# Optimization experiments

Measured on AMD Instinct MI355X. Metric: run time of the kernel, lower is better.

The kernel has to match this reference:

```python
import jax, jax.numpy as jnp
import numpy as np

B, T, I, H, O = 128, 512, 64, 1024, 12

def setup_inputs() -> dict:
    key = jax.random.key(0)
    ks = jax.random.split(key, 7)
    s_ih = 1.0 / np.sqrt(H)
    return {
        "x": jax.random.normal(ks[0], (B, T, I), dtype=jnp.float32),
        "W_ih": jax.random.normal(ks[1], (H, I), dtype=jnp.float32) * s_ih,
        "W_hh": jax.random.normal(ks[2], (H, H), dtype=jnp.float32) * s_ih,
        "b_ih": jax.random.normal(ks[3], (H,), dtype=jnp.float32) * s_ih,
        "b_hh": jax.random.normal(ks[4], (H,), dtype=jnp.float32) * s_ih,
        "W_out": jax.random.normal(ks[5], (O, H), dtype=jnp.float32) * s_ih,
        "b_out": jax.random.normal(ks[6], (O,), dtype=jnp.float32) * s_ih,
    }

def reference(x, W_ih, W_hh, b_ih, b_hh, W_out, b_out):
    # x: [B, T, I] (batch_first). Vanilla tanh RNN, h0 = 0.
    Bn, Tn, _ = x.shape
    Hn = W_hh.shape[0]
    # Precompute input projections for all timesteps (batched GEMM).
    xp = jnp.einsum('bti,hi->tbh', x, W_ih) + b_ih + b_hh  # [T, B, H]
    h0 = jnp.zeros((Bn, Hn), dtype=x.dtype)

    def step(h, xt):
        h_new = jnp.tanh(xt + h @ W_hh.T)
        return h_new, h_new

    _, hs = jax.lax.scan(step, h0, xp)  # hs: [T, B, H]
    hs = jnp.swapaxes(hs, 0, 1)         # [B, T, H]
    out = jnp.einsum('bth,oh->bto', hs, W_out) + b_out  # [B, T, O]
    return out.reshape(-1, 12)
```

## Files before the change

### kernel.cpp

```cpp
#include <hip/hip_runtime.h>
#include <hip/hip_bf16.h>

#define B_ 128
#define T_ 512
#define I_ 64
#define H_ 1024
#define O_ 12
#define HSTEP (H_ * B_)
#define XSTEP (I_ * B_)
#define RSLOT 16384
#define TIMEOUT 2000

typedef __attribute__((ext_vector_type(8))) short bf16x8;
typedef __attribute__((ext_vector_type(4))) float f32x4;

#define MFMA16 __builtin_amdgcn_mfma_f32_16x16x32_bf16

__device__ __forceinline__ float bf2f(unsigned short s) {
  unsigned u = ((unsigned)s) << 16; float f; __builtin_memcpy(&f, &u, 4); return f;
}
__device__ __forceinline__ unsigned short f2bf(float f) {
  unsigned u; __builtin_memcpy(&u, &f, 4);
  u += 0x7fffu + ((u >> 16) & 1u);
  return (unsigned short)(u >> 16);
}

__device__ __forceinline__ unsigned ldA32(const unsigned* p) {
  return __hip_atomic_load(p, __ATOMIC_RELAXED, __HIP_MEMORY_SCOPE_AGENT);
}
__device__ __forceinline__ void stA32(unsigned* p, unsigned v) {
  __hip_atomic_store(p, v, __ATOMIC_RELAXED, __HIP_MEMORY_SCOPE_AGENT);
}
__device__ __forceinline__ unsigned long long ldA64(const unsigned long long* p) {
  return __hip_atomic_load(p, __ATOMIC_RELAXED, __HIP_MEMORY_SCOPE_AGENT);
}

__device__ __forceinline__ void store32_sc0(unsigned* p, unsigned v) {
  asm volatile("global_store_dword %0, %1, off sc0" :: "v"(p), "v"(v) : "memory");
}
__device__ __forceinline__ unsigned poll_sc0(const unsigned* p) {
  unsigned v;
  asm volatile("global_load_dword %0, %1, off sc0\n\ts_waitcnt vmcnt(0)"
               : "=v"(v) : "v"(p) : "memory");
  return v;
}
__device__ __forceinline__ bf16x8 load16_sc0(const void* p) {
  bf16x8 v;
  asm volatile("global_load_dwordx4 %0, %1, off sc0" : "=v"(v) : "v"(p));
  return v;
}
__device__ __forceinline__ void waitv8(bf16x8& v0, bf16x8& v1, bf16x8& v2, bf16x8& v3,
                                       bf16x8& v4, bf16x8& v5, bf16x8& v6, bf16x8& v7) {
  asm volatile("s_waitcnt vmcnt(0)"
               : "+v"(v0), "+v"(v1), "+v"(v2), "+v"(v3),
                 "+v"(v4), "+v"(v5), "+v"(v6), "+v"(v7) :: "memory");
}

__global__ void prep_xp(const float* __restrict__ x,
                        unsigned short* __restrict__ xPhi) {
  const int t = blockIdx.x;
  for (int u = threadIdx.x; u < 1024; u += 256) {
    const int ib = u >> 7, b = u & 127;
    const float* src = x + ((size_t)b * T_ + t) * I_ + ib * 8;
    bf16x8 hi;
    #pragma unroll
    for (int j = 0; j < 8; ++j) hi[j] = (short)f2bf(src[j]);
    *(bf16x8*)(xPhi + ((size_t)t * 1024 + u) * 8) = hi;
  }
}

__global__ void prep_misc(const float* __restrict__ W_out, float* __restrict__ WoT,
                          unsigned* __restrict__ bar) {
  const int idx = blockIdx.x * 256 + threadIdx.x;
  if (idx < 1024) bar[idx] = 0u;
  const int k = idx >> 4, s = idx & 15;
  float v = 0.0f;
  if (s < 6)                 v = W_out[s * H_ + k];
  else if (s >= 8 && s < 14) v = W_out[(s - 2) * H_ + k];
  WoT[idx] = v;
}

__global__ __launch_bounds__(256, 1) void rnn_mfma(
    const float* __restrict__ W_ih, const float* __restrict__ W_hh,
    const float* __restrict__ b_ih, const float* __restrict__ b_hh,
    const unsigned short* __restrict__ xPhi, unsigned short* __restrict__ hP,
    unsigned short* __restrict__ rF, unsigned short* __restrict__ rS,
    unsigned* __restrict__ bar)
{
  __shared__ float part[4][544];
  __shared__ float biasS[32];
  __shared__ unsigned modeS;
  const int tid = threadIdx.x, bid = blockIdx.x;
  const int wave = tid >> 6, lane = tid & 63, quad = lane >> 4, ln = lane & 15;
  const int g = bid & 7, rg = bid >> 3;
  const int r0 = rg * 32, b0 = g * 16;
  if (tid < 32) biasS[tid] = b_ih[r0 + tid] + b_hh[r0 + tid];
  if (tid == 0) modeS = 1u;

  bf16x8 ahhi[2][8], ahlo[2][8];
  #pragma unroll
  for (int mt = 0; mt < 2; ++mt)
    #pragma unroll
    for (int kt = 0; kt < 8; ++kt) {
      const float* wp = W_hh + (size_t)(r0 + mt * 16 + ln) * H_
                        + wave * 256 + kt * 32 + quad * 8;
      #pragma unroll
      for (int j = 0; j < 8; ++j) {
        float v = wp[j];
        unsigned short h = f2bf(v);
        ahhi[mt][kt][j] = (short)h;
        ahlo[mt][kt][j] = (short)f2bf(v - bf2f(h));
      }
    }
  bf16x8 axhi[2], axlo[2];
  if (wave < 2)
    #pragma unroll
    for (int mt = 0; mt < 2; ++mt) {
      const float* wp = W_ih + (size_t)(r0 + mt * 16 + ln) * I_
                        + wave * 32 + quad * 8;
      #pragma unroll
      for (int j = 0; j < 8; ++j) {
        float v = wp[j];
        unsigned short h = f2bf(v);
        axhi[mt][j] = (short)h;
        axlo[mt][j] = (short)f2bf(v - bf2f(h));
      }
    }
  __syncthreads();
  unsigned mode = 1u;

  const int bcol = b0 + ln;
  unsigned short* rFg = rF + (size_t)g * 2 * RSLOT;
  unsigned short* rSg = rS + (size_t)g * 2 * RSLOT;

  f32x4 xacc0 = {0.f, 0.f, 0.f, 0.f}, xacc1 = {0.f, 0.f, 0.f, 0.f};
  auto computeX = [&](int t) {
    if (wave < 2) {
      const size_t xo = (((size_t)t * 8 + wave * 4 + quad) * B_ + bcol) * 8;
      bf16x8 bxh = *(const bf16x8*)(xPhi + xo);
      f32x4 t0 = {0.f, 0.f, 0.f, 0.f}, t1 = {0.f, 0.f, 0.f, 0.f};
      t0 = MFMA16(axhi[0], bxh, t0, 0, 0, 0);
      t0 = MFMA16(axlo[0], bxh, t0, 0, 0, 0);
      t1 = MFMA16(axhi[1], bxh, t1, 0, 0, 0);
      t1 = MFMA16(axlo[1], bxh, t1, 0, 0, 0);
      xacc0 = t0; xacc1 = t1;
    }
  };
  computeX(0);

  for (int t = 0; t < T_; ++t) {
    f32x4 accA0 = xacc0, accA1 = xacc1;
    f32x4 accB0 = {0.f, 0.f, 0.f, 0.f}, accB1 = {0.f, 0.f, 0.f, 0.f};

    if (t > 0) {
      const int soff = ((wave * 32 + quad) * 16 + ln) * 8;
      bf16x8 bh[8];
      if (mode) {
        const unsigned short* slot = rFg + ((t - 1) & 1) * RSLOT + soff;
        #pragma unroll
        for (int kt = 0; kt < 8; ++kt)
          bh[kt] = load16_sc0(slot + kt * 512);
        waitv8(bh[0], bh[1], bh[2], bh[3], bh[4], bh[5], bh[6], bh[7]);
      } else {
        const unsigned long long* slot =
            (const unsigned long long*)(rSg + ((t - 1) & 1) * RSLOT + soff);
        #pragma unroll
        for (int kt = 0; kt < 8; ++kt) {
          union { unsigned long long u[2]; bf16x8 v; } U;
          U.u[0] = ldA64(slot + kt * 128);
          U.u[1] = ldA64(slot + kt * 128 + 1);
          bh[kt] = U.v;
        }
      }
      #pragma unroll
      for (int kt = 0; kt < 8; ++kt) {
        accA0 = MFMA16(ahhi[0][kt], bh[kt], accA0, 0, 0, 0);
        accA1 = MFMA16(ahhi[1][kt], bh[kt], accA1, 0, 0, 0);
        accB0 = MFMA16(ahlo[0][kt], bh[kt], accB0, 0, 0, 0);
        accB1 = MFMA16(ahlo[1][kt], bh[kt], accB1, 0, 0, 0);
      }
    }

    #pragma unroll
    for (int r = 0; r < 4; ++r) {
      part[wave][r * 68 + lane]       = accA0[r] + accB0[r];
      part[wave][(4 + r) * 68 + lane] = accA1[r] + accB1[r];
    }
    __syncthreads();

    {
      const int n = tid & 15, rp = tid >> 4;
      const int m0 = rp * 2;
      unsigned short o[2];
      #pragma unroll
      for (int rr = 0; rr < 2; ++rr) {
        const int m = m0 + rr;
        const int f = ((m >> 4) * 4 + (m & 3)) * 68 + ((m >> 2) & 3) * 16 + n;
        float s = part[0][f] + part[1][f] + part[2][f] + part[3][f] + biasS[m];
        o[rr] = f2bf(tanhf(s));
      }
      const unsigned pk = (unsigned)o[0] | ((unsigned)o[1] << 16);
      const int R = r0 + m0;
      *(unsigned*)(hP + (size_t)t * HSTEP
                   + ((size_t)(R >> 3) * B_ + (b0 + n)) * 8 + (R & 7)) = pk;
      const int soff = ((R >> 3) * 16 + n) * 8 + (R & 7);
      store32_sc0((unsigned*)(rFg + (t & 1) * RSLOT + soff), pk);
      stA32      ((unsigned*)(rSg + (t & 1) * RSLOT + soff), pk);
    }

    if (t < T_ - 1) {
      computeX(t + 1);
      asm volatile("s_waitcnt vmcnt(0)" ::: "memory");
      __syncthreads();
      if (tid == 0) {
        store32_sc0(&bar[g * 32 + rg],      (unsigned)(t + 1));
        stA32      (&bar[256 + g * 32 + rg], (unsigned)(t + 1));
      }
      if (tid < 64) {
        int ok = 0;
        if (mode) {
          for (int it = 0; it < TIMEOUT && !ok; ++it) {
            unsigned v = (lane < 32) ? poll_sc0(&bar[g * 32 + lane]) : 0xffffffffu;
            ok = __all((int)(v >= (unsigned)(t + 1)));
          }
        }
        if (!ok) {
          if (tid == 0) modeS = 0u;
          for (;;) {
            unsigned v = (lane < 32) ? ldA32(&bar[256 + g * 32 + lane]) : 0xffffffffu;
            if (__all((int)(v >= (unsigned)(t + 1)))) break;
            __builtin_amdgcn_s_sleep(1);
          }
        }
      }
      __syncthreads();
      mode = modeS;
    }
  }
}

__global__ __launch_bounds__(256, 2) void out_proj(
    const unsigned short* __restrict__ hP, const float* __restrict__ WoT,
    const float* __restrict__ b_out, float* __restrict__ out)
{
  const int t = blockIdx.x;
  const int tid = threadIdx.x;
  const int b  = tid & 127;
  const int oh = tid >> 7;
  float a0 = b_out[oh * 6 + 0], a1 = b_out[oh * 6 + 1], a2 = b_out[oh * 6 + 2];
  float a3 = b_out[oh * 6 + 3], a4 = b_out[oh * 6 + 4], a5 = b_out[oh * 6 + 5];
  const unsigned short* hp = hP + (size_t)t * HSTEP + (size_t)b * 8;
  const float4* W4 = (const float4*)WoT;
  for (int kb = 0; kb < 128; ++kb) {
    bf16x8 hv = *(const bf16x8*)(hp + (size_t)kb * (B_ * 8));
    #pragma unroll
    for (int j = 0; j < 8; ++j) {
      const int k = kb * 8 + j;
      float h = bf2f((unsigned short)hv[j]);
      float4 wa = W4[k * 4 + oh * 2];
      float4 wb = W4[k * 4 + oh * 2 + 1];
      a0 += wa.x * h; a1 += wa.y * h; a2 += wa.z * h;
      a3 += wa.w * h; a4 += wb.x * h; a5 += wb.y * h;
    }
  }
  float* op = out + ((size_t)b * T_ + t) * O_ + oh * 6;
  op[0] = a0; op[1] = a1; op[2] = a2; op[3] = a3; op[4] = a4; op[5] = a5;
}

extern "C" void kernel_launch(void* const* d_in, const int* in_sizes, int n_in,
                              void* d_out, int out_size, void* d_ws, size_t ws_size,
                              hipStream_t stream)
{
  const float* x     = (const float*)d_in[0];
  const float* W_ih  = (const float*)d_in[1];
  const float* W_hh  = (const float*)d_in[2];
  const float* b_ih  = (const float*)d_in[3];
  const float* b_hh  = (const float*)d_in[4];
  const float* W_out = (const float*)d_in[5];
  const float* b_out = (const float*)d_in[6];
  float* out = (float*)d_out;

  unsigned short* hP   = (unsigned short*)d_ws;
  unsigned short* xPhi = hP + (size_t)T_ * HSTEP;
  float*          WoT  = (float*)(xPhi + (size_t)T_ * XSTEP);
  unsigned short* rF   = (unsigned short*)(WoT + (size_t)H_ * 16);
  unsigned short* rS   = rF + (size_t)8 * 2 * RSLOT;
  unsigned*       bar  = (unsigned*)(rS + (size_t)8 * 2 * RSLOT);

  prep_xp  <<<T_,  256, 0, stream>>>(x, xPhi);
  prep_misc<<<64,  256, 0, stream>>>(W_out, WoT, bar);
  rnn_mfma <<<256, 256, 0, stream>>>(W_ih, W_hh, b_ih, b_hh, xPhi, hP, rF, rS, bar);
  out_proj <<<T_,  256, 0, stream>>>(hP, WoT, b_out, out);
}
```

Before: 1.895 ms.

## Stage hidden-state output in LDS and split stores, flag and polling across waves

The tanh outputs are first packed into a shared staging buffer. Each exchange copy is then written with wide 16-byte stores by a dedicated wave, and that wave raises its own barrier flag right after its stores drain. The history store to hP goes to another wave, and a fourth wave polls for the other blocks in parallel. This is meant to shorten the per-timestep critical path of the persistent recurrent loop by removing the block-wide sync before the flag write and overlapping computeX with polling. The catch is that computeX(t+1) is now issued from two waves (0 and 1), which may duplicate or split that work depending on how computeX is written internally.

```diff
diff --git a/kernel.cpp b/kernel.cpp
--- a/kernel.cpp
+++ b/kernel.cpp
@@ -13,6 +13,7 @@
 
 typedef __attribute__((ext_vector_type(8))) short bf16x8;
 typedef __attribute__((ext_vector_type(4))) float f32x4;
+typedef __attribute__((ext_vector_type(4))) unsigned u32x4;
 
 #define MFMA16 __builtin_amdgcn_mfma_f32_16x16x32_bf16
 
@@ -34,9 +35,15 @@
 __device__ __forceinline__ unsigned long long ldA64(const unsigned long long* p) {
   return __hip_atomic_load(p, __ATOMIC_RELAXED, __HIP_MEMORY_SCOPE_AGENT);
 }
+__device__ __forceinline__ void stA64(unsigned long long* p, unsigned long long v) {
+  __hip_atomic_store(p, v, __ATOMIC_RELAXED, __HIP_MEMORY_SCOPE_AGENT);
+}
 
 __device__ __forceinline__ void store32_sc0(unsigned* p, unsigned v) {
   asm volatile("global_store_dword %0, %1, off sc0" :: "v"(p), "v"(v) : "memory");
+}
+__device__ __forceinline__ void store16_sc0(void* p, u32x4 v) {
+  asm volatile("global_store_dwordx4 %0, %1, off sc0" :: "v"(p), "v"(v) : "memory");
 }
 __device__ __forceinline__ unsigned poll_sc0(const unsigned* p) {
   unsigned v;
@@ -54,6 +61,9 @@
   asm volatile("s_waitcnt vmcnt(0)"
                : "+v"(v0), "+v"(v1), "+v"(v2), "+v"(v3),
                  "+v"(v4), "+v"(v5), "+v"(v6), "+v"(v7) :: "memory");
+}
+__device__ __forceinline__ void vmwait0() {
+  asm volatile("s_waitcnt vmcnt(0)" ::: "memory");
 }
 
 __global__ void prep_xp(const float* __restrict__ x,
@@ -88,6 +98,7 @@
     unsigned* __restrict__ bar)
 {
   __shared__ float part[4][544];
+  __shared__ unsigned stage[256];
   __shared__ float biasS[32];
   __shared__ unsigned modeS;
   const int tid = threadIdx.x, bid = blockIdx.x;
@@ -199,43 +210,50 @@
         float s = part[0][f] + part[1][f] + part[2][f] + part[3][f] + biasS[m];
         o[rr] = f2bf(tanhf(s));
       }
-      const unsigned pk = (unsigned)o[0] | ((unsigned)o[1] << 16);
-      const int R = r0 + m0;
-      *(unsigned*)(hP + (size_t)t * HSTEP
-                   + ((size_t)(R >> 3) * B_ + (b0 + n)) * 8 + (R & 7)) = pk;
-      const int soff = ((R >> 3) * 16 + n) * 8 + (R & 7);
-      store32_sc0((unsigned*)(rFg + (t & 1) * RSLOT + soff), pk);
-      stA32      ((unsigned*)(rSg + (t & 1) * RSLOT + soff), pk);
-    }
-
-    if (t < T_ - 1) {
-      computeX(t + 1);
-      asm volatile("s_waitcnt vmcnt(0)" ::: "memory");
-      __syncthreads();
-      if (tid == 0) {
-        store32_sc0(&bar[g * 32 + rg],      (unsigned)(t + 1));
-        stA32      (&bar[256 + g * 32 + rg], (unsigned)(t + 1));
-      }
-      if (tid < 64) {
-        int ok = 0;
-        if (mode) {
-          for (int it = 0; it < TIMEOUT && !ok; ++it) {
-            unsigned v = (lane < 32) ? poll_sc0(&bar[g * 32 + lane]) : 0xffffffffu;
-            ok = __all((int)(v >= (unsigned)(t + 1)));
-          }
+      stage[(rp >> 2) * 64 + n * 4 + (rp & 3)] =
+          (unsigned)o[0] | ((unsigned)o[1] << 16);
+    }
+    __syncthreads();
+
+    const int slotoff = (t & 1) * RSLOT;
+    if (wave == 0) {
+      u32x4 v = *(const u32x4*)&stage[lane * 4];
+      store16_sc0(rFg + slotoff + rg * 512 + lane * 8, v);
+      vmwait0();
+      if (lane == 0 && t < T_ - 1) store32_sc0(&bar[g * 32 + rg], (unsigned)(t + 1));
+      if (t < T_ - 1) computeX(t + 1);
+    } else if (wave == 1) {
+      const unsigned long long* s = (const unsigned long long*)&stage[lane * 4];
+      unsigned long long* d =
+          (unsigned long long*)(rSg + slotoff + rg * 512) + lane * 2;
+      stA64(d, s[0]); stA64(d + 1, s[1]);
+      vmwait0();
+      if (lane == 0 && t < T_ - 1) stA32(&bar[256 + g * 32 + rg], (unsigned)(t + 1));
+      if (t < T_ - 1) computeX(t + 1);
+    } else if (wave == 2) {
+      u32x4 v = *(const u32x4*)&stage[lane * 4];
+      *(u32x4*)(hP + (size_t)t * HSTEP
+                + ((size_t)(rg * 4 + (lane >> 4)) * B_ + b0 + (lane & 15)) * 8) = v;
+      vmwait0();
+    } else if (t < T_ - 1) {
+      int ok = 0;
+      if (mode) {
+        for (int it = 0; it < TIMEOUT && !ok; ++it) {
+          unsigned v = (lane < 32) ? poll_sc0(&bar[g * 32 + lane]) : 0xffffffffu;
+          ok = __all((int)(v >= (unsigned)(t + 1)));
         }
-        if (!ok) {
-          if (tid == 0) modeS = 0u;
-          for (;;) {
-            unsigned v = (lane < 32) ? ldA32(&bar[256 + g * 32 + lane]) : 0xffffffffu;
-            if (__all((int)(v >= (unsigned)(t + 1)))) break;
-            __builtin_amdgcn_s_sleep(1);
-          }
+      }
+      if (!ok) {
+        if (lane == 0) modeS = 0u;
+        for (;;) {
+          unsigned v = (lane < 32) ? ldA32(&bar[256 + g * 32 + lane]) : 0xffffffffu;
+          if (__all((int)(v >= (unsigned)(t + 1)))) break;
+          __builtin_amdgcn_s_sleep(1);
         }
       }
-      __syncthreads();
-      mode = modeS;
-    }
+    }
+    __syncthreads();
+    mode = modeS;
   }
 }
 
```

Result: no change. 1.907 ms (+0.6%).
